# Kernel tuning notes

Hardware: AMD Instinct MI355X
Metric: run time of the kernel (lower is better)

Reference implementation:

```python
import jax, jax.numpy as jnp
import numpy as np
import math

D_MODEL, HEADS, KQ = 1024, 16, 64
B, S = 2, 2048

def setup_inputs() -> dict:
    key = jax.random.key(0)
    k1, k2, k3, k4, k5 = jax.random.split(key, 5)
    scale = D_MODEL ** (-0.5)
    return {
        "x_BSE": jax.random.normal(k1, (B, S, D_MODEL), dtype=jnp.float32),
        "w_q": jax.random.normal(k2, (D_MODEL, HEADS, KQ), dtype=jnp.float32) * scale,
        "w_k": jax.random.normal(k3, (D_MODEL, HEADS, KQ), dtype=jnp.float32) * scale,
        "w_v": jax.random.normal(k4, (D_MODEL, HEADS, KQ), dtype=jnp.float32) * scale,
        "w_o": jax.random.normal(k5, (D_MODEL, HEADS, KQ), dtype=jnp.float32) * scale,
    }

def reference(x_BSE, w_q, w_k, w_v, w_o):
    # QKV projections (self-attention: memory = x)
    q_BSHK = jnp.einsum('BSE,EHK->BSHK', x_BSE, w_q)
    k_BMHK = jnp.einsum('BSE,EHK->BSHK', x_BSE, w_k)
    v_BMHK = jnp.einsum('BSE,EHK->BSHK', x_BSE, w_v)
    logits_BSHM = jnp.einsum('BSHK,BMHK->BSHM', q_BSHK, k_BMHK) / math.sqrt(KQ)
    # causal (diagonal) mask: query position >= memory position
    Sdim, Mdim = logits_BSHM.shape[1], logits_BSHM.shape[3]
    qpos = jnp.arange(Sdim)[:, None]          # [S,1]
    mpos = jnp.arange(Mdim)[None, :]          # [1,M]
    mask_SM = jnp.where(qpos >= mpos, 0.0, -jnp.inf).astype(logits_BSHM.dtype)
    logits_BSHM = logits_BSHM + mask_SM[None, :, None, :]
    probs_BSHM = jax.nn.softmax(logits_BSHM, axis=3)
    out_BSHK = jnp.einsum('BSHM,BMHK->BSHK', probs_BSHM, v_BMHK)
    return jnp.einsum('BSHK,EHK->BSE', out_BSHK, w_o)
```

## Files before the change

### kernel.cpp

```cpp
#include <hip/hip_runtime.h>
#include <hip/hip_bf16.h>

typedef __attribute__((ext_vector_type(4)))  float f32x4;
typedef __attribute__((ext_vector_type(16))) float f32x16;
typedef __attribute__((ext_vector_type(8)))  short short8;
typedef __attribute__((ext_vector_type(4)))  short short4v;

__device__ __forceinline__ short f2bf(float f) {
  union { float f; unsigned u; } x; x.f = f;
  unsigned r = (x.u + 0x7FFFu + ((x.u >> 16) & 1u)) >> 16;
  return (short)r;
}
__device__ __forceinline__ unsigned pk2(float lo, float hi) {
  return (unsigned)(unsigned short)f2bf(lo) | ((unsigned)(unsigned short)f2bf(hi) << 16);
}

__global__ __launch_bounds__(256) void k_cast(const float* __restrict__ in,
                                              short* __restrict__ out, int n4) {
  int i = blockIdx.x * 256 + threadIdx.x;
  if (i >= n4) return;
  f32x4 v = ((const f32x4*)in)[i];
  short4v s;
  s[0] = f2bf(v[0]); s[1] = f2bf(v[1]); s[2] = f2bf(v[2]); s[3] = f2bf(v[3]);
  ((short4v*)out)[i] = s;
}

__global__ __launch_bounds__(256) void k_pack(const float* __restrict__ wq,
                                              const float* __restrict__ wk,
                                              const float* __restrict__ wv,
                                              short* __restrict__ WT) {
  int nt = blockIdx.x, et = blockIdx.y, sel = blockIdx.z;
  const float* w = sel == 0 ? wq : (sel == 1 ? wk : wv);
  __shared__ float tile[64][65];
  int tid = threadIdx.x;
  int cl = tid & 63, rw = tid >> 6;
#pragma unroll
  for (int j = 0; j < 16; ++j) {
    int el = j * 4 + rw;
    tile[el][cl] = w[(size_t)(et * 64 + el) * 1024 + nt * 64 + cl];
  }
  __syncthreads();
#pragma unroll
  for (int j = 0; j < 16; ++j) {
    int nl = j * 4 + rw;
    int n = sel * 1024 + nt * 64 + nl;
    WT[(size_t)n * 1024 + et * 64 + cl] = f2bf(tile[cl][nl]);
  }
}

template <int EPI>
__global__ __launch_bounds__(256) void k_gemm(const short* __restrict__ A,
                                              const short* __restrict__ B,
                                              short* __restrict__ Qo, short* __restrict__ Ko,
                                              short* __restrict__ Vo, float* __restrict__ out,
                                              int M, int N, int K) {
  __shared__ short As[128][40];
  __shared__ short Bs[128][40];
  int tid = threadIdx.x;
  int bm = blockIdx.y * 128, bn = blockIdx.x * 128;
  int wid = tid >> 6, lane = tid & 63;
  int wm = (wid >> 1) * 64, wn = (wid & 1) * 64;
  int lg = lane >> 4, lr = lane & 15;
  f32x4 acc[4][4] = {};

  int sr = tid >> 2, sc = tid & 3;
  const short* Ar0 = A + (size_t)(bm + sr) * K;
  const short* Ar1 = A + (size_t)(bm + sr + 64) * K;
  const short* Br0 = B + (size_t)(bn + sr) * K;
  const short* Br1 = B + (size_t)(bn + sr + 64) * K;

  short8 pa0 = *(const short8*)&Ar0[sc * 8];
  short8 pa1 = *(const short8*)&Ar1[sc * 8];
  short8 pb0 = *(const short8*)&Br0[sc * 8];
  short8 pb1 = *(const short8*)&Br1[sc * 8];

  int nk = K >> 5;
  for (int kt = 0; kt < nk; ++kt) {
    __syncthreads();
    *(short8*)&As[sr][sc * 8] = pa0;
    *(short8*)&As[sr + 64][sc * 8] = pa1;
    *(short8*)&Bs[sr][sc * 8] = pb0;
    *(short8*)&Bs[sr + 64][sc * 8] = pb1;
    if (kt + 1 < nk) {
      int ko = (kt + 1) * 32;
      pa0 = *(const short8*)&Ar0[ko + sc * 8];
      pa1 = *(const short8*)&Ar1[ko + sc * 8];
      pb0 = *(const short8*)&Br0[ko + sc * 8];
      pb1 = *(const short8*)&Br1[ko + sc * 8];
    }
    __syncthreads();
    short8 af[4], bf_[4];
#pragma unroll
    for (int mt = 0; mt < 4; ++mt)
      af[mt] = *(const short8*)&As[wm + mt * 16 + lr][lg * 8];
#pragma unroll
    for (int ntl = 0; ntl < 4; ++ntl)
      bf_[ntl] = *(const short8*)&Bs[wn + ntl * 16 + lr][lg * 8];
#pragma unroll
    for (int mt = 0; mt < 4; ++mt)
#pragma unroll
      for (int ntl = 0; ntl < 4; ++ntl)
        acc[mt][ntl] = __builtin_amdgcn_mfma_f32_16x16x32_bf16(af[mt], bf_[ntl], acc[mt][ntl], 0, 0, 0);
  }

#pragma unroll
  for (int mt = 0; mt < 4; ++mt)
#pragma unroll
    for (int ntl = 0; ntl < 4; ++ntl)
#pragma unroll
      for (int rr = 0; rr < 4; ++rr) {
        int m = bm + wm + mt * 16 + lg * 4 + rr;
        int n = bn + wn + ntl * 16 + lr;
        float val = acc[mt][ntl][rr];
        if (EPI == 0) {
          int b = m >> 11, s = m & 2047;
          int sel = n >> 10, hk = n & 1023;
          int h = hk >> 6, kd = hk & 63;
          if (sel == 0) Qo[((size_t)(b * 16 + h) * 2048 + s) * 64 + kd] = f2bf(val * 0.125f);
          else if (sel == 1) Ko[((size_t)(b * 16 + h) * 2048 + s) * 64 + kd] = f2bf(val);
          else Vo[((size_t)(b * 16 + h) * 64 + kd) * 2048 + s] = f2bf(val);
        } else {
          out[(size_t)m * 1024 + n] = val;
        }
      }
}

__global__ __launch_bounds__(256) void k_attn(const short* __restrict__ Q,
                                              const short* __restrict__ K,
                                              const short* __restrict__ VT,
                                              short* __restrict__ O) {
  const int S = 2048;
  int bh = blockIdx.x, a = blockIdx.y;
  int wid = threadIdx.x >> 6, lane = threadIdx.x & 63;
  int qw = (wid & 2) ? (63 - 2 * a - (wid & 1)) : (2 * a + (wid & 1));
  int q0 = qw * 32;
  int hi = lane >> 5, ln = lane & 31;
  int q_g = q0 + ln;

  const short* Qb = Q + (size_t)bh * S * 64;
  const short* Kb = K + (size_t)bh * S * 64;
  const short* Vb = VT + (size_t)bh * 64 * S;

  short8 qf[4];
#pragma unroll
  for (int ds = 0; ds < 4; ++ds)
    qf[ds] = *(const short8*)&Qb[(size_t)q_g * 64 + ds * 16 + hi * 8];

  f32x16 acoA = {}, acoB = {};
  float m = -1e30f, l = 0.f;

  int ntile = qw + 1;
  short8 kc[4], kn[4];
#pragma unroll
  for (int ds = 0; ds < 4; ++ds)
    kc[ds] = *(const short8*)&Kb[(size_t)ln * 64 + ds * 16 + hi * 8];

  for (int t = 0; t < ntile; ++t) {
    const size_t vro = (size_t)ln * S + t * 32 + hi * 8;
    short8 v00 = *(const short8*)&Vb[vro];
    short8 v01 = *(const short8*)&Vb[vro + 16];
    short8 v10 = *(const short8*)&Vb[vro + (size_t)32 * S];
    short8 v11 = *(const short8*)&Vb[vro + (size_t)32 * S + 16];
    if (t + 1 < ntile) {
#pragma unroll
      for (int ds = 0; ds < 4; ++ds)
        kn[ds] = *(const short8*)&Kb[(size_t)((t + 1) * 32 + ln) * 64 + ds * 16 + hi * 8];
    }

    f32x16 sa = {};
#pragma unroll
    for (int ds = 0; ds < 4; ++ds)
      sa = __builtin_amdgcn_mfma_f32_32x32x16_bf16(kc[ds], qf[ds], sa, 0, 0, 0);

    if (t == qw) {
#pragma unroll
      for (int r = 0; r < 16; ++r) {
        int kv_g = t * 32 + (r & 3) + 8 * (r >> 2) + 4 * hi;
        if (kv_g > q_g) sa[r] = -1e30f;
      }
    }

    float x0 = fmaxf(sa[0], sa[1]),  x1 = fmaxf(sa[2], sa[3]);
    float x2 = fmaxf(sa[4], sa[5]),  x3 = fmaxf(sa[6], sa[7]);
    float x4 = fmaxf(sa[8], sa[9]),  x5 = fmaxf(sa[10], sa[11]);
    float x6 = fmaxf(sa[12], sa[13]), x7 = fmaxf(sa[14], sa[15]);
    x0 = fmaxf(x0, x1); x2 = fmaxf(x2, x3); x4 = fmaxf(x4, x5); x6 = fmaxf(x6, x7);
    x0 = fmaxf(x0, x2); x4 = fmaxf(x4, x6);
    float mx = fmaxf(x0, x4);
    mx = fmaxf(mx, __shfl_xor(mx, 32));

    float mnew = fmaxf(m, mx);
    float alpha = __expf(m - mnew);
    m = mnew;

    float p[16];
#pragma unroll
    for (int r = 0; r < 16; ++r) p[r] = __expf(sa[r] - mnew);
    float s0 = (p[0] + p[1]) + (p[2] + p[3]);
    float s1 = (p[4] + p[5]) + (p[6] + p[7]);
    float s2 = (p[8] + p[9]) + (p[10] + p[11]);
    float s3 = (p[12] + p[13]) + (p[14] + p[15]);
    float rsum = (s0 + s1) + (s2 + s3);
    rsum += __shfl_xor(rsum, 32);
    l = l * alpha + rsum;
    acoA *= alpha;
    acoB *= alpha;

#pragma unroll
    for (int s = 0; s < 2; ++s) {
      unsigned c0 = pk2(p[8 * s + 0], p[8 * s + 1]);
      unsigned c1 = pk2(p[8 * s + 2], p[8 * s + 3]);
      unsigned c2 = pk2(p[8 * s + 4], p[8 * s + 5]);
      unsigned c3 = pk2(p[8 * s + 6], p[8 * s + 7]);
      unsigned pc0 = (unsigned)__shfl_xor((int)c0, 32);
      unsigned pc1 = (unsigned)__shfl_xor((int)c1, 32);
      unsigned pc2 = (unsigned)__shfl_xor((int)c2, 32);
      unsigned pc3 = (unsigned)__shfl_xor((int)c3, 32);
      union { unsigned u[4]; short8 v; } pb;
      pb.u[0] = hi ? pc2 : c0;
      pb.u[1] = hi ? pc3 : c1;
      pb.u[2] = hi ? c2 : pc0;
      pb.u[3] = hi ? c3 : pc1;
      if (s == 0) {
        acoA = __builtin_amdgcn_mfma_f32_32x32x16_bf16(v00, pb.v, acoA, 0, 0, 0);
        acoB = __builtin_amdgcn_mfma_f32_32x32x16_bf16(v10, pb.v, acoB, 0, 0, 0);
      } else {
        acoA = __builtin_amdgcn_mfma_f32_32x32x16_bf16(v01, pb.v, acoA, 0, 0, 0);
        acoB = __builtin_amdgcn_mfma_f32_32x32x16_bf16(v11, pb.v, acoB, 0, 0, 0);
      }
    }
#pragma unroll
    for (int ds = 0; ds < 4; ++ds) kc[ds] = kn[ds];
  }

  float rl = 1.f / l;
  int b = bh >> 4, h = bh & 15;
  size_t obase = ((size_t)b * 2048 + q_g) * 1024 + h * 64;
#pragma unroll
  for (int g = 0; g < 4; ++g) {
    int d0 = 8 * g + 4 * hi;
    unsigned uA0 = pk2(acoA[4 * g] * rl, acoA[4 * g + 1] * rl);
    unsigned uA1 = pk2(acoA[4 * g + 2] * rl, acoA[4 * g + 3] * rl);
    unsigned uB0 = pk2(acoB[4 * g] * rl, acoB[4 * g + 1] * rl);
    unsigned uB1 = pk2(acoB[4 * g + 2] * rl, acoB[4 * g + 3] * rl);
    *(unsigned*)&O[obase + d0] = uA0;
    *(unsigned*)&O[obase + d0 + 2] = uA1;
    *(unsigned*)&O[obase + 32 + d0] = uB0;
    *(unsigned*)&O[obase + 32 + d0 + 2] = uB1;
  }
}

extern "C" void kernel_launch(void* const* d_in, const int* in_sizes, int n_in,
                              void* d_out, int out_size, void* d_ws, size_t ws_size,
                              hipStream_t stream) {
  const float* x  = (const float*)d_in[0];
  const float* wq = (const float*)d_in[1];
  const float* wk = (const float*)d_in[2];
  const float* wv = (const float*)d_in[3];
  const float* wo = (const float*)d_in[4];
  float* out = (float*)d_out;
  char* ws = (char*)d_ws;

  short* x_bf  = (short*)(ws);
  short* WqkvT = (short*)(ws + ((size_t)8 << 20));
  short* wo_bf = (short*)(ws + ((size_t)14 << 20));
  short* Qb    = (short*)(ws + ((size_t)16 << 20));
  short* Kb    = (short*)(ws + ((size_t)24 << 20));
  short* Vt    = (short*)(ws + ((size_t)32 << 20));
  short* Ob    = (short*)(ws + ((size_t)40 << 20));

  k_cast<<<4096, 256, 0, stream>>>(x, x_bf, 1048576);
  k_cast<<<1024, 256, 0, stream>>>(wo, wo_bf, 262144);
  k_pack<<<dim3(16, 16, 3), 256, 0, stream>>>(wq, wk, wv, WqkvT);
  k_gemm<0><<<dim3(24, 32), 256, 0, stream>>>(x_bf, WqkvT, Qb, Kb, Vt, nullptr, 4096, 3072, 1024);
  k_attn<<<dim3(32, 16), 256, 0, stream>>>(Qb, Kb, Vt, Ob);
  k_gemm<1><<<dim3(8, 32), 256, 0, stream>>>(Ob, wo_bf, nullptr, nullptr, nullptr, out, 4096, 1024, 1024);
}
```

Baseline: 149.2 us.

## Split attention KV range across two waves per query tile and merge partials

Attention now splits each query tile's causal KV range into two halves processed by separate waves. Each wave writes an unnormalized bf16 partial output plus its running max and sum, and a new merge kernel combines the halves. The grid doubles and launch bounds request higher occupancy. Q is prescaled by log2(e)/sqrt(d) so the softmax uses exp2f. The split is meant to balance causal work and raise parallelism, at the cost of an extra kernel launch, extra memory traffic for the partials, and bf16 rounding of the unnormalized partials.

```diff
diff --git a/kernel.cpp b/kernel.cpp
--- a/kernel.cpp
+++ b/kernel.cpp
@@ -10,6 +10,10 @@
   union { float f; unsigned u; } x; x.f = f;
   unsigned r = (x.u + 0x7FFFu + ((x.u >> 16) & 1u)) >> 16;
   return (short)r;
+}
+__device__ __forceinline__ float bf2f(short s) {
+  union { unsigned u; float f; } x; x.u = ((unsigned)(unsigned short)s) << 16;
+  return x.f;
 }
 __device__ __forceinline__ unsigned pk2(float lo, float hi) {
   return (unsigned)(unsigned short)f2bf(lo) | ((unsigned)(unsigned short)f2bf(hi) << 16);
@@ -116,7 +120,7 @@
           int b = m >> 11, s = m & 2047;
           int sel = n >> 10, hk = n & 1023;
           int h = hk >> 6, kd = hk & 63;
-          if (sel == 0) Qo[((size_t)(b * 16 + h) * 2048 + s) * 64 + kd] = f2bf(val * 0.125f);
+          if (sel == 0) Qo[((size_t)(b * 16 + h) * 2048 + s) * 64 + kd] = f2bf(val * 0.18033688011112042f);
           else if (sel == 1) Ko[((size_t)(b * 16 + h) * 2048 + s) * 64 + kd] = f2bf(val);
           else Vo[((size_t)(b * 16 + h) * 64 + kd) * 2048 + s] = f2bf(val);
         } else {
@@ -125,17 +129,29 @@
       }
 }
 
-__global__ __launch_bounds__(256) void k_attn(const short* __restrict__ Q,
-                                              const short* __restrict__ K,
-                                              const short* __restrict__ VT,
-                                              short* __restrict__ O) {
+__global__ __launch_bounds__(256, 4) void k_attn(const short* __restrict__ Q,
+                                                 const short* __restrict__ K,
+                                                 const short* __restrict__ VT,
+                                                 short* __restrict__ P0,
+                                                 short* __restrict__ P1,
+                                                 float* __restrict__ ML) {
   const int S = 2048;
   int bh = blockIdx.x, a = blockIdx.y;
+  int kk = a >> 3, a0 = a & 7;
+  int c = (kk == 0) ? (a0 + 1) : (kk == 1) ? (16 - a0) : (kk == 2) ? (17 + a0) : (32 - a0);
   int wid = threadIdx.x >> 6, lane = threadIdx.x & 63;
-  int qw = (wid & 2) ? (63 - 2 * a - (wid & 1)) : (2 * a + (wid & 1));
-  int q0 = qw * 32;
+  int qw, half;
+  if (wid == 0)      { qw = 2 * c - 2;       half = 0; }
+  else if (wid == 1) { qw = 2 * c - 1;       half = 0; }
+  else if (wid == 2) { qw = 2 * c - 1;       half = 1; }
+  else               { qw = (2 * c) & 63;    half = 1; }
+  int nt_total = qw + 1;
+  int nt0 = (nt_total + 1) >> 1;
+  int tb = half ? nt0 : 0;
+  int te = half ? nt_total : nt0;
+
   int hi = lane >> 5, ln = lane & 31;
-  int q_g = q0 + ln;
+  int q_g = qw * 32 + ln;
 
   const short* Qb = Q + (size_t)bh * S * 64;
   const short* Kb = K + (size_t)bh * S * 64;
@@ -149,105 +165,135 @@
   f32x16 acoA = {}, acoB = {};
   float m = -1e30f, l = 0.f;
 
-  int ntile = qw + 1;
-  short8 kc[4], kn[4];
-#pragma unroll
-  for (int ds = 0; ds < 4; ++ds)
-    kc[ds] = *(const short8*)&Kb[(size_t)ln * 64 + ds * 16 + hi * 8];
-
-  for (int t = 0; t < ntile; ++t) {
-    const size_t vro = (size_t)ln * S + t * 32 + hi * 8;
-    short8 v00 = *(const short8*)&Vb[vro];
-    short8 v01 = *(const short8*)&Vb[vro + 16];
-    short8 v10 = *(const short8*)&Vb[vro + (size_t)32 * S];
-    short8 v11 = *(const short8*)&Vb[vro + (size_t)32 * S + 16];
-    if (t + 1 < ntile) {
+  if (tb < te) {
+    short8 kc[4], kn[4];
+#pragma unroll
+    for (int ds = 0; ds < 4; ++ds)
+      kc[ds] = *(const short8*)&Kb[(size_t)(tb * 32 + ln) * 64 + ds * 16 + hi * 8];
+
+    for (int t = tb; t < te; ++t) {
+      const size_t vro = (size_t)ln * S + t * 32 + hi * 8;
+      short8 v00 = *(const short8*)&Vb[vro];
+      short8 v01 = *(const short8*)&Vb[vro + 16];
+      short8 v10 = *(const short8*)&Vb[vro + (size_t)32 * S];
+      short8 v11 = *(const short8*)&Vb[vro + (size_t)32 * S + 16];
+      if (t + 1 < te) {
+#pragma unroll
+        for (int ds = 0; ds < 4; ++ds)
+          kn[ds] = *(const short8*)&Kb[(size_t)((t + 1) * 32 + ln) * 64 + ds * 16 + hi * 8];
+      }
+
+      f32x16 sa = {};
 #pragma unroll
       for (int ds = 0; ds < 4; ++ds)
-        kn[ds] = *(const short8*)&Kb[(size_t)((t + 1) * 32 + ln) * 64 + ds * 16 + hi * 8];
+        sa = __builtin_amdgcn_mfma_f32_32x32x16_bf16(kc[ds], qf[ds], sa, 0, 0, 0);
+
+      if (t == qw) {
+#pragma unroll
+        for (int r = 0; r < 16; ++r) {
+          int kv_g = t * 32 + (r & 3) + 8 * (r >> 2) + 4 * hi;
+          if (kv_g > q_g) sa[r] = -1e30f;
+        }
+      }
+
+      float x0 = fmaxf(sa[0], sa[1]),  x1 = fmaxf(sa[2], sa[3]);
+      float x2 = fmaxf(sa[4], sa[5]),  x3 = fmaxf(sa[6], sa[7]);
+      float x4 = fmaxf(sa[8], sa[9]),  x5 = fmaxf(sa[10], sa[11]);
+      float x6 = fmaxf(sa[12], sa[13]), x7 = fmaxf(sa[14], sa[15]);
+      x0 = fmaxf(x0, x1); x2 = fmaxf(x2, x3); x4 = fmaxf(x4, x5); x6 = fmaxf(x6, x7);
+      x0 = fmaxf(x0, x2); x4 = fmaxf(x4, x6);
+      float mx = fmaxf(x0, x4);
+      mx = fmaxf(mx, __shfl_xor(mx, 32));
+
+      float mnew = fmaxf(m, mx);
+      float alpha = exp2f(m - mnew);
+      m = mnew;
+
+      float p[16];
+#pragma unroll
+      for (int r = 0; r < 16; ++r) p[r] = exp2f(sa[r] - mnew);
+      float s0 = (p[0] + p[1]) + (p[2] + p[3]);
+      float s1 = (p[4] + p[5]) + (p[6] + p[7]);
+      float s2 = (p[8] + p[9]) + (p[10] + p[11]);
+      float s3 = (p[12] + p[13]) + (p[14] + p[15]);
+      float rsum = (s0 + s1) + (s2 + s3);
+      rsum += __shfl_xor(rsum, 32);
+      l = l * alpha + rsum;
+      acoA *= alpha;
+      acoB *= alpha;
+
+#pragma unroll
+      for (int s = 0; s < 2; ++s) {
+        unsigned c0 = pk2(p[8 * s + 0], p[8 * s + 1]);
+        unsigned c1 = pk2(p[8 * s + 2], p[8 * s + 3]);
+        unsigned c2 = pk2(p[8 * s + 4], p[8 * s + 5]);
+        unsigned c3 = pk2(p[8 * s + 6], p[8 * s + 7]);
+        unsigned pc0 = (unsigned)__shfl_xor((int)c0, 32);
+        unsigned pc1 = (unsigned)__shfl_xor((int)c1, 32);
+        unsigned pc2 = (unsigned)__shfl_xor((int)c2, 32);
+        unsigned pc3 = (unsigned)__shfl_xor((int)c3, 32);
+        union { unsigned u[4]; short8 v; } pb;
+        pb.u[0] = hi ? pc2 : c0;
+        pb.u[1] = hi ? pc3 : c1;
+        pb.u[2] = hi ? c2 : pc0;
+        pb.u[3] = hi ? c3 : pc1;
+        if (s == 0) {
+          acoA = __builtin_amdgcn_mfma_f32_32x32x16_bf16(v00, pb.v, acoA, 0, 0, 0);
+          acoB = __builtin_amdgcn_mfma_f32_32x32x16_bf16(v10, pb.v, acoB, 0, 0, 0);
+        } else {
+          acoA = __builtin_amdgcn_mfma_f32_32x32x16_bf16(v01, pb.v, acoA, 0, 0, 0);
+          acoB = __builtin_amdgcn_mfma_f32_32x32x16_bf16(v11, pb.v, acoB, 0, 0, 0);
+        }
+      }
+#pragma unroll
+      for (int ds = 0; ds < 4; ++ds) kc[ds] = kn[ds];
     }
-
-    f32x16 sa = {};
-#pragma unroll
-    for (int ds = 0; ds < 4; ++ds)
-      sa = __builtin_amdgcn_mfma_f32_32x32x16_bf16(kc[ds], qf[ds], sa, 0, 0, 0);
-
-    if (t == qw) {
-#pragma unroll
-      for (int r = 0; r < 16; ++r) {
-        int kv_g = t * 32 + (r & 3) + 8 * (r >> 2) + 4 * hi;
-        if (kv_g > q_g) sa[r] = -1e30f;
-      }
-    }
-
-    float x0 = fmaxf(sa[0], sa[1]),  x1 = fmaxf(sa[2], sa[3]);
-    float x2 = fmaxf(sa[4], sa[5]),  x3 = fmaxf(sa[6], sa[7]);
-    float x4 = fmaxf(sa[8], sa[9]),  x5 = fmaxf(sa[10], sa[11]);
-    float x6 = fmaxf(sa[12], sa[13]), x7 = fmaxf(sa[14], sa[15]);
-    x0 = fmaxf(x0, x1); x2 = fmaxf(x2, x3); x4 = fmaxf(x4, x5); x6 = fmaxf(x6, x7);
-    x0 = fmaxf(x0, x2); x4 = fmaxf(x4, x6);
-    float mx = fmaxf(x0, x4);
-    mx = fmaxf(mx, __shfl_xor(mx, 32));
-
-    float mnew = fmaxf(m, mx);
-    float alpha = __expf(m - mnew);
-    m = mnew;
-
-    float p[16];
-#pragma unroll
-    for (int r = 0; r < 16; ++r) p[r] = __expf(sa[r] - mnew);
-    float s0 = (p[0] + p[1]) + (p[2] + p[3]);
-    float s1 = (p[4] + p[5]) + (p[6] + p[7]);
-    float s2 = (p[8] + p[9]) + (p[10] + p[11]);
-    float s3 = (p[12] + p[13]) + (p[14] + p[15]);
-    float rsum = (s0 + s1) + (s2 + s3);
-    rsum += __shfl_xor(rsum, 32);
-    l = l * alpha + rsum;
-    acoA *= alpha;
-    acoB *= alpha;
-
-#pragma unroll
-    for (int s = 0; s < 2; ++s) {
-      unsigned c0 = pk2(p[8 * s + 0], p[8 * s + 1]);
-      unsigned c1 = pk2(p[8 * s + 2], p[8 * s + 3]);
-      unsigned c2 = pk2(p[8 * s + 4], p[8 * s + 5]);
-      unsigned c3 = pk2(p[8 * s + 6], p[8 * s + 7]);
-      unsigned pc0 = (unsigned)__shfl_xor((int)c0, 32);
-      unsigned pc1 = (unsigned)__shfl_xor((int)c1, 32);
-      unsigned pc2 = (unsigned)__shfl_xor((int)c2, 32);
-      unsigned pc3 = (unsigned)__shfl_xor((int)c3, 32);
-      union { unsigned u[4]; short8 v; } pb;
-      pb.u[0] = hi ? pc2 : c0;
-      pb.u[1] = hi ? pc3 : c1;
-      pb.u[2] = hi ? c2 : pc0;
-      pb.u[3] = hi ? c3 : pc1;
-      if (s == 0) {
-        acoA = __builtin_amdgcn_mfma_f32_32x32x16_bf16(v00, pb.v, acoA, 0, 0, 0);
-        acoB = __builtin_amdgcn_mfma_f32_32x32x16_bf16(v10, pb.v, acoB, 0, 0, 0);
-      } else {
-        acoA = __builtin_amdgcn_mfma_f32_32x32x16_bf16(v01, pb.v, acoA, 0, 0, 0);
-        acoB = __builtin_amdgcn_mfma_f32_32x32x16_bf16(v11, pb.v, acoB, 0, 0, 0);
-      }
-    }
-#pragma unroll
-    for (int ds = 0; ds < 4; ++ds) kc[ds] = kn[ds];
-  }
-
-  float rl = 1.f / l;
-  int b = bh >> 4, h = bh & 15;
-  size_t obase = ((size_t)b * 2048 + q_g) * 1024 + h * 64;
+  }
+
+  int row = (bh << 11) + q_g;
+  ML[row * 4 + half * 2 + 0] = m;
+  ML[row * 4 + half * 2 + 1] = l;
+  short* Op = half ? P1 : P0;
+  size_t base = (size_t)row * 64;
 #pragma unroll
   for (int g = 0; g < 4; ++g) {
     int d0 = 8 * g + 4 * hi;
-    unsigned uA0 = pk2(acoA[4 * g] * rl, acoA[4 * g + 1] * rl);
-    unsigned uA1 = pk2(acoA[4 * g + 2] * rl, acoA[4 * g + 3] * rl);
-    unsigned uB0 = pk2(acoB[4 * g] * rl, acoB[4 * g + 1] * rl);
-    unsigned uB1 = pk2(acoB[4 * g + 2] * rl, acoB[4 * g + 3] * rl);
-    *(unsigned*)&O[obase + d0] = uA0;
-    *(unsigned*)&O[obase + d0 + 2] = uA1;
-    *(unsigned*)&O[obase + 32 + d0] = uB0;
-    *(unsigned*)&O[obase + 32 + d0 + 2] = uB1;
-  }
+    *(unsigned*)&Op[base + d0]          = pk2(acoA[4 * g], acoA[4 * g + 1]);
+    *(unsigned*)&Op[base + d0 + 2]      = pk2(acoA[4 * g + 2], acoA[4 * g + 3]);
+    *(unsigned*)&Op[base + 32 + d0]     = pk2(acoB[4 * g], acoB[4 * g + 1]);
+    *(unsigned*)&Op[base + 32 + d0 + 2] = pk2(acoB[4 * g + 2], acoB[4 * g + 3]);
+  }
+}
+
+__global__ __launch_bounds__(256) void k_merge(const short* __restrict__ P0,
+                                               const short* __restrict__ P1,
+                                               const float* __restrict__ ML,
+                                               short* __restrict__ O) {
+  int gi = blockIdx.x * 256 + threadIdx.x;
+  int row = gi >> 2;
+  int dc = (gi & 3) << 4;
+  float m0 = ML[row * 4 + 0], l0 = ML[row * 4 + 1];
+  float m1 = ML[row * 4 + 2], l1 = ML[row * 4 + 3];
+  float M = fmaxf(m0, m1);
+  float w0 = exp2f(m0 - M), w1 = exp2f(m1 - M);
+  float rL = 1.f / (l0 * w0 + l1 * w1);
+  w0 *= rL; w1 *= rL;
+  size_t pbase = (size_t)row * 64 + dc;
+  short8 a0 = *(const short8*)&P0[pbase];
+  short8 a1 = *(const short8*)&P0[pbase + 8];
+  short8 b0 = *(const short8*)&P1[pbase];
+  short8 b1 = *(const short8*)&P1[pbase + 8];
+  int bh = row >> 11, q = row & 2047;
+  int b = bh >> 4, h = bh & 15;
+  size_t obase = ((size_t)b * 2048 + q) * 1024 + h * 64 + dc;
+  short8 o0, o1;
+#pragma unroll
+  for (int j = 0; j < 8; ++j) {
+    o0[j] = f2bf(bf2f(a0[j]) * w0 + bf2f(b0[j]) * w1);
+    o1[j] = f2bf(bf2f(a1[j]) * w0 + bf2f(b1[j]) * w1);
+  }
+  *(short8*)&O[obase] = o0;
+  *(short8*)&O[obase + 8] = o1;
 }
 
 extern "C" void kernel_launch(void* const* d_in, const int* in_sizes, int n_in,
@@ -268,11 +314,15 @@
   short* Kb    = (short*)(ws + ((size_t)24 << 20));
   short* Vt    = (short*)(ws + ((size_t)32 << 20));
   short* Ob    = (short*)(ws + ((size_t)40 << 20));
+  short* P0    = (short*)(ws);
+  float* ML    = (float*)(ws + ((size_t)8 << 20));
+  short* P1    = (short*)(ws + ((size_t)48 << 20));
 
   k_cast<<<4096, 256, 0, stream>>>(x, x_bf, 1048576);
   k_cast<<<1024, 256, 0, stream>>>(wo, wo_bf, 262144);
   k_pack<<<dim3(16, 16, 3), 256, 0, stream>>>(wq, wk, wv, WqkvT);
   k_gemm<0><<<dim3(24, 32), 256, 0, stream>>>(x_bf, WqkvT, Qb, Kb, Vt, nullptr, 4096, 3072, 1024);
-  k_attn<<<dim3(32, 16), 256, 0, stream>>>(Qb, Kb, Vt, Ob);
+  k_attn<<<dim3(32, 32), 256, 0, stream>>>(Qb, Kb, Vt, P0, P1, ML);
+  k_merge<<<1024, 256, 0, stream>>>(P0, P1, ML, Ob);
   k_gemm<1><<<dim3(8, 32), 256, 0, stream>>>(Ob, wo_bf, nullptr, nullptr, nullptr, out, 4096, 1024, 1024);
 }
```

After: 151.9 us. No clear change (+1.8%).

## Share K/V tiles via swizzled LDS double buffer in attention with 2-wave blocks

Applied to the files above, without the earlier changes.

The attention kernel now uses 128-thread blocks where two adjacent query tiles cooperatively stage K and V tiles into a double-buffered, XOR-swizzled shared-memory buffer, instead of each wave loading K/V directly from global memory. It also folds log2(e) into the Q scale so exp2f replaces __expf, skips the accumulator rescale when the running max does not change, and uses the hardware v_cvt_pk_bf16_f32 instruction for packing. The aim is to cut redundant global K/V traffic and per-tile ALU work, at the cost of a __syncthreads per tile and an idle wave on the final diagonal tile. Block pairing is reordered to balance causal work.

```diff
diff --git a/kernel.cpp b/kernel.cpp
--- a/kernel.cpp
+++ b/kernel.cpp
@@ -11,8 +11,10 @@
   unsigned r = (x.u + 0x7FFFu + ((x.u >> 16) & 1u)) >> 16;
   return (short)r;
 }
-__device__ __forceinline__ unsigned pk2(float lo, float hi) {
-  return (unsigned)(unsigned short)f2bf(lo) | ((unsigned)(unsigned short)f2bf(hi) << 16);
+__device__ __forceinline__ unsigned cvtpk(float lo, float hi) {
+  unsigned r;
+  asm("v_cvt_pk_bf16_f32 %0, %1, %2" : "=v"(r) : "v"(lo), "v"(hi));
+  return r;
 }
 
 __global__ __launch_bounds__(256) void k_cast(const float* __restrict__ in,
@@ -116,7 +118,7 @@
           int b = m >> 11, s = m & 2047;
           int sel = n >> 10, hk = n & 1023;
           int h = hk >> 6, kd = hk & 63;
-          if (sel == 0) Qo[((size_t)(b * 16 + h) * 2048 + s) * 64 + kd] = f2bf(val * 0.125f);
+          if (sel == 0) Qo[((size_t)(b * 16 + h) * 2048 + s) * 64 + kd] = f2bf(val * 0.18033688011112042f);
           else if (sel == 1) Ko[((size_t)(b * 16 + h) * 2048 + s) * 64 + kd] = f2bf(val);
           else Vo[((size_t)(b * 16 + h) * 64 + kd) * 2048 + s] = f2bf(val);
         } else {
@@ -125,17 +127,26 @@
       }
 }
 
-__global__ __launch_bounds__(256) void k_attn(const short* __restrict__ Q,
-                                              const short* __restrict__ K,
-                                              const short* __restrict__ VT,
-                                              short* __restrict__ O) {
+__global__ __launch_bounds__(128, 2) void k_attn(const short* __restrict__ Q,
+                                                 const short* __restrict__ K,
+                                                 const short* __restrict__ VT,
+                                                 short* __restrict__ O) {
   const int S = 2048;
-  int bh = blockIdx.x, a = blockIdx.y;
-  int wid = threadIdx.x >> 6, lane = threadIdx.x & 63;
-  int qw = (wid & 2) ? (63 - 2 * a - (wid & 1)) : (2 * a + (wid & 1));
-  int q0 = qw * 32;
+  int bh = blockIdx.x;
+  int y = blockIdx.y;
+  int y0 = y & 7, sel = y >> 3;
+  int g = (sel == 0) ? y0 : (sel == 1) ? (15 - y0) : (sel == 2) ? (16 + y0) : (31 - y0);
+
+  int tid = threadIdx.x;
+  int wid = tid >> 6, lane = tid & 63;
   int hi = lane >> 5, ln = lane & 31;
-  int q_g = q0 + ln;
+  int qw = 2 * g + wid;
+  int ntile = qw + 1;
+  int tmax = 2 * g + 2;
+  int q_g = qw * 32 + ln;
+
+  __shared__ short Ks[2][32][64];
+  __shared__ short Vs[2][64][32];
 
   const short* Qb = Q + (size_t)bh * S * 64;
   const short* Kb = K + (size_t)bh * S * 64;
@@ -146,107 +157,125 @@
   for (int ds = 0; ds < 4; ++ds)
     qf[ds] = *(const short8*)&Qb[(size_t)q_g * 64 + ds * 16 + hi * 8];
 
+  int kr = tid >> 2, kcb = tid & 3;
+  int vd = tid >> 1, vcb = tid & 1;
+  const short* kgp = Kb + (size_t)kr * 64;
+  const short* vgp = Vb + (size_t)vd * S;
+
+  short8 kreg0 = *(const short8*)&kgp[(size_t)0 + kcb * 8];
+  short8 kreg1 = *(const short8*)&kgp[(size_t)0 + (kcb + 4) * 8];
+  short8 vreg0 = *(const short8*)&vgp[(size_t)0 + vcb * 8];
+  short8 vreg1 = *(const short8*)&vgp[(size_t)0 + (vcb + 2) * 8];
+
   f32x16 acoA = {}, acoB = {};
   float m = -1e30f, l = 0.f;
 
-  int ntile = qw + 1;
-  short8 kc[4], kn[4];
-#pragma unroll
-  for (int ds = 0; ds < 4; ++ds)
-    kc[ds] = *(const short8*)&Kb[(size_t)ln * 64 + ds * 16 + hi * 8];
-
-  for (int t = 0; t < ntile; ++t) {
-    const size_t vro = (size_t)ln * S + t * 32 + hi * 8;
-    short8 v00 = *(const short8*)&Vb[vro];
-    short8 v01 = *(const short8*)&Vb[vro + 16];
-    short8 v10 = *(const short8*)&Vb[vro + (size_t)32 * S];
-    short8 v11 = *(const short8*)&Vb[vro + (size_t)32 * S + 16];
-    if (t + 1 < ntile) {
-#pragma unroll
-      for (int ds = 0; ds < 4; ++ds)
-        kn[ds] = *(const short8*)&Kb[(size_t)((t + 1) * 32 + ln) * 64 + ds * 16 + hi * 8];
+  for (int t = 0; t < tmax; ++t) {
+    int buf = t & 1;
+    *(short8*)&Ks[buf][kr][(kcb ^ (kr & 7)) * 8]       = kreg0;
+    *(short8*)&Ks[buf][kr][((kcb + 4) ^ (kr & 7)) * 8] = kreg1;
+    *(short8*)&Vs[buf][vd][(vcb ^ (vd & 3)) * 8]       = vreg0;
+    *(short8*)&Vs[buf][vd][((vcb + 2) ^ (vd & 3)) * 8] = vreg1;
+    if (t + 1 < tmax) {
+      size_t ko = (size_t)(t + 1) * 32 * 64;
+      size_t vo = (size_t)(t + 1) * 32;
+      kreg0 = *(const short8*)&kgp[ko + kcb * 8];
+      kreg1 = *(const short8*)&kgp[ko + (kcb + 4) * 8];
+      vreg0 = *(const short8*)&vgp[vo + vcb * 8];
+      vreg1 = *(const short8*)&vgp[vo + (vcb + 2) * 8];
     }
-
-    f32x16 sa = {};
-#pragma unroll
-    for (int ds = 0; ds < 4; ++ds)
-      sa = __builtin_amdgcn_mfma_f32_32x32x16_bf16(kc[ds], qf[ds], sa, 0, 0, 0);
-
-    if (t == qw) {
-#pragma unroll
-      for (int r = 0; r < 16; ++r) {
-        int kv_g = t * 32 + (r & 3) + 8 * (r >> 2) + 4 * hi;
-        if (kv_g > q_g) sa[r] = -1e30f;
+    __syncthreads();
+
+    if (t < ntile) {
+      short8 kc0 = *(const short8*)&Ks[buf][ln][((0 + hi) ^ (ln & 7)) * 8];
+      short8 kc1 = *(const short8*)&Ks[buf][ln][((2 + hi) ^ (ln & 7)) * 8];
+      short8 kc2 = *(const short8*)&Ks[buf][ln][((4 + hi) ^ (ln & 7)) * 8];
+      short8 kc3 = *(const short8*)&Ks[buf][ln][((6 + hi) ^ (ln & 7)) * 8];
+      f32x16 sa = {};
+      sa = __builtin_amdgcn_mfma_f32_32x32x16_bf16(kc0, qf[0], sa, 0, 0, 0);
+      sa = __builtin_amdgcn_mfma_f32_32x32x16_bf16(kc1, qf[1], sa, 0, 0, 0);
+      sa = __builtin_amdgcn_mfma_f32_32x32x16_bf16(kc2, qf[2], sa, 0, 0, 0);
+      sa = __builtin_amdgcn_mfma_f32_32x32x16_bf16(kc3, qf[3], sa, 0, 0, 0);
+
+      if (t == qw) {
+#pragma unroll
+        for (int r = 0; r < 16; ++r) {
+          int kv_g = t * 32 + (r & 3) + 8 * (r >> 2) + 4 * hi;
+          if (kv_g > q_g) sa[r] = -1e30f;
+        }
+      }
+
+      short8 v00 = *(const short8*)&Vs[buf][ln][((0 + hi) ^ (ln & 3)) * 8];
+      short8 v01 = *(const short8*)&Vs[buf][ln][((2 + hi) ^ (ln & 3)) * 8];
+      short8 v10 = *(const short8*)&Vs[buf][32 + ln][((0 + hi) ^ (ln & 3)) * 8];
+      short8 v11 = *(const short8*)&Vs[buf][32 + ln][((2 + hi) ^ (ln & 3)) * 8];
+
+      float x0 = fmaxf(sa[0], sa[1]),  x1 = fmaxf(sa[2], sa[3]);
+      float x2 = fmaxf(sa[4], sa[5]),  x3 = fmaxf(sa[6], sa[7]);
+      float x4 = fmaxf(sa[8], sa[9]),  x5 = fmaxf(sa[10], sa[11]);
+      float x6 = fmaxf(sa[12], sa[13]), x7 = fmaxf(sa[14], sa[15]);
+      x0 = fmaxf(x0, x1); x2 = fmaxf(x2, x3); x4 = fmaxf(x4, x5); x6 = fmaxf(x6, x7);
+      x0 = fmaxf(x0, x2); x4 = fmaxf(x4, x6);
+      float mx = fmaxf(x0, x4);
+      mx = fmaxf(mx, __shfl_xor(mx, 32));
+
+      float mnew = fmaxf(m, mx);
+      float p[16];
+#pragma unroll
+      for (int r = 0; r < 16; ++r) p[r] = exp2f(sa[r] - mnew);
+      float s0 = (p[0] + p[1]) + (p[2] + p[3]);
+      float s1 = (p[4] + p[5]) + (p[6] + p[7]);
+      float s2 = (p[8] + p[9]) + (p[10] + p[11]);
+      float s3 = (p[12] + p[13]) + (p[14] + p[15]);
+      float rsum = (s0 + s1) + (s2 + s3);
+      rsum += __shfl_xor(rsum, 32);
+
+      if (__all(mx <= m)) {
+        l += rsum;
+      } else {
+        float alpha = exp2f(m - mnew);
+        m = mnew;
+        l = l * alpha + rsum;
+        acoA *= alpha;
+        acoB *= alpha;
+      }
+
+#pragma unroll
+      for (int s = 0; s < 2; ++s) {
+        unsigned c0 = cvtpk(p[8 * s + 0], p[8 * s + 1]);
+        unsigned c1 = cvtpk(p[8 * s + 2], p[8 * s + 3]);
+        unsigned c2 = cvtpk(p[8 * s + 4], p[8 * s + 5]);
+        unsigned c3 = cvtpk(p[8 * s + 6], p[8 * s + 7]);
+        unsigned pc0 = (unsigned)__shfl_xor((int)c0, 32);
+        unsigned pc1 = (unsigned)__shfl_xor((int)c1, 32);
+        unsigned pc2 = (unsigned)__shfl_xor((int)c2, 32);
+        unsigned pc3 = (unsigned)__shfl_xor((int)c3, 32);
+        union { unsigned u[4]; short8 v; } pb;
+        pb.u[0] = hi ? pc2 : c0;
+        pb.u[1] = hi ? pc3 : c1;
+        pb.u[2] = hi ? c2 : pc0;
+        pb.u[3] = hi ? c3 : pc1;
+        if (s == 0) {
+          acoA = __builtin_amdgcn_mfma_f32_32x32x16_bf16(v00, pb.v, acoA, 0, 0, 0);
+          acoB = __builtin_amdgcn_mfma_f32_32x32x16_bf16(v10, pb.v, acoB, 0, 0, 0);
+        } else {
+          acoA = __builtin_amdgcn_mfma_f32_32x32x16_bf16(v01, pb.v, acoA, 0, 0, 0);
+          acoB = __builtin_amdgcn_mfma_f32_32x32x16_bf16(v11, pb.v, acoB, 0, 0, 0);
+        }
       }
     }
-
-    float x0 = fmaxf(sa[0], sa[1]),  x1 = fmaxf(sa[2], sa[3]);
-    float x2 = fmaxf(sa[4], sa[5]),  x3 = fmaxf(sa[6], sa[7]);
-    float x4 = fmaxf(sa[8], sa[9]),  x5 = fmaxf(sa[10], sa[11]);
-    float x6 = fmaxf(sa[12], sa[13]), x7 = fmaxf(sa[14], sa[15]);
-    x0 = fmaxf(x0, x1); x2 = fmaxf(x2, x3); x4 = fmaxf(x4, x5); x6 = fmaxf(x6, x7);
-    x0 = fmaxf(x0, x2); x4 = fmaxf(x4, x6);
-    float mx = fmaxf(x0, x4);
-    mx = fmaxf(mx, __shfl_xor(mx, 32));
-
-    float mnew = fmaxf(m, mx);
-    float alpha = __expf(m - mnew);
-    m = mnew;
-
-    float p[16];
-#pragma unroll
-    for (int r = 0; r < 16; ++r) p[r] = __expf(sa[r] - mnew);
-    float s0 = (p[0] + p[1]) + (p[2] + p[3]);
-    float s1 = (p[4] + p[5]) + (p[6] + p[7]);
-    float s2 = (p[8] + p[9]) + (p[10] + p[11]);
-    float s3 = (p[12] + p[13]) + (p[14] + p[15]);
-    float rsum = (s0 + s1) + (s2 + s3);
-    rsum += __shfl_xor(rsum, 32);
-    l = l * alpha + rsum;
-    acoA *= alpha;
-    acoB *= alpha;
-
-#pragma unroll
-    for (int s = 0; s < 2; ++s) {
-      unsigned c0 = pk2(p[8 * s + 0], p[8 * s + 1]);
-      unsigned c1 = pk2(p[8 * s + 2], p[8 * s + 3]);
-      unsigned c2 = pk2(p[8 * s + 4], p[8 * s + 5]);
-      unsigned c3 = pk2(p[8 * s + 6], p[8 * s + 7]);
-      unsigned pc0 = (unsigned)__shfl_xor((int)c0, 32);
-      unsigned pc1 = (unsigned)__shfl_xor((int)c1, 32);
-      unsigned pc2 = (unsigned)__shfl_xor((int)c2, 32);
-      unsigned pc3 = (unsigned)__shfl_xor((int)c3, 32);
-      union { unsigned u[4]; short8 v; } pb;
-      pb.u[0] = hi ? pc2 : c0;
-      pb.u[1] = hi ? pc3 : c1;
-      pb.u[2] = hi ? c2 : pc0;
-      pb.u[3] = hi ? c3 : pc1;
-      if (s == 0) {
-        acoA = __builtin_amdgcn_mfma_f32_32x32x16_bf16(v00, pb.v, acoA, 0, 0, 0);
-        acoB = __builtin_amdgcn_mfma_f32_32x32x16_bf16(v10, pb.v, acoB, 0, 0, 0);
-      } else {
-        acoA = __builtin_amdgcn_mfma_f32_32x32x16_bf16(v01, pb.v, acoA, 0, 0, 0);
-        acoB = __builtin_amdgcn_mfma_f32_32x32x16_bf16(v11, pb.v, acoB, 0, 0, 0);
-      }
-    }
-#pragma unroll
-    for (int ds = 0; ds < 4; ++ds) kc[ds] = kn[ds];
   }
 
   float rl = 1.f / l;
   int b = bh >> 4, h = bh & 15;
   size_t obase = ((size_t)b * 2048 + q_g) * 1024 + h * 64;
 #pragma unroll
-  for (int g = 0; g < 4; ++g) {
-    int d0 = 8 * g + 4 * hi;
-    unsigned uA0 = pk2(acoA[4 * g] * rl, acoA[4 * g + 1] * rl);
-    unsigned uA1 = pk2(acoA[4 * g + 2] * rl, acoA[4 * g + 3] * rl);
-    unsigned uB0 = pk2(acoB[4 * g] * rl, acoB[4 * g + 1] * rl);
-    unsigned uB1 = pk2(acoB[4 * g + 2] * rl, acoB[4 * g + 3] * rl);
-    *(unsigned*)&O[obase + d0] = uA0;
-    *(unsigned*)&O[obase + d0 + 2] = uA1;
-    *(unsigned*)&O[obase + 32 + d0] = uB0;
-    *(unsigned*)&O[obase + 32 + d0 + 2] = uB1;
+  for (int g4 = 0; g4 < 4; ++g4) {
+    int d0 = 8 * g4 + 4 * hi;
+    *(unsigned*)&O[obase + d0]          = cvtpk(acoA[4 * g4] * rl, acoA[4 * g4 + 1] * rl);
+    *(unsigned*)&O[obase + d0 + 2]      = cvtpk(acoA[4 * g4 + 2] * rl, acoA[4 * g4 + 3] * rl);
+    *(unsigned*)&O[obase + 32 + d0]     = cvtpk(acoB[4 * g4] * rl, acoB[4 * g4 + 1] * rl);
+    *(unsigned*)&O[obase + 32 + d0 + 2] = cvtpk(acoB[4 * g4 + 2] * rl, acoB[4 * g4 + 3] * rl);
   }
 }
 
@@ -273,6 +302,6 @@
   k_cast<<<1024, 256, 0, stream>>>(wo, wo_bf, 262144);
   k_pack<<<dim3(16, 16, 3), 256, 0, stream>>>(wq, wk, wv, WqkvT);
   k_gemm<0><<<dim3(24, 32), 256, 0, stream>>>(x_bf, WqkvT, Qb, Kb, Vt, nullptr, 4096, 3072, 1024);
-  k_attn<<<dim3(32, 16), 256, 0, stream>>>(Qb, Kb, Vt, Ob);
+  k_attn<<<dim3(32, 32), 128, 0, stream>>>(Qb, Kb, Vt, Ob);
   k_gemm<1><<<dim3(8, 32), 256, 0, stream>>>(Ob, wo_bf, nullptr, nullptr, nullptr, out, 4096, 1024, 1024);
 }
```

Result: faster. 145.6 us (-2.4%).
